# Optimization experiments

Measured on AMD Instinct MI355X. Metric: run time of the kernel, lower is better.

The kernel has to match this reference:

```python
import jax, jax.numpy as jnp
import numpy as np
import jax.lax as lax

EPS = 1e-5

def conv3x3(x, w):
    # x: [B,C,H,W], w: [O,C,3,3], stride 1, padding 1
    return lax.conv_general_dilated(x, w, (1, 1), ((1, 1), (1, 1)),
                                    dimension_numbers=('NCHW', 'OIHW', 'NCHW'))

def bn(x, s, b, m, v):
    inv = s / jnp.sqrt(v + EPS)
    return x * inv[None, :, None, None] + (b - m * inv)[None, :, None, None]

def conv_bn_relu(x, w, s, b, m, v):
    return jax.nn.relu(bn(conv3x3(x, w), s, b, m, v))

def spatial_attention(x, q_w, q_b, v_w, v_b, gamma):
    # Self_attention: q_conv used for both q and k (k_conv is dead in source)
    B, C, H, W = x.shape
    N = H * W
    q = (jnp.einsum('bchw,oc->bohw', x, q_w) + q_b[None, :, None, None]).reshape(B, -1, N)  # [B,Cq,N]
    v = (jnp.einsum('bchw,oc->bohw', x, v_w) + v_b[None, :, None, None]).reshape(B, C, N)   # [B,C,N]
    energy = jnp.einsum('bcn,bcm->bnm', q, q)          # [B,N,N]
    attn = jax.nn.softmax(energy, axis=-1)
    out = jnp.einsum('bcm,bnm->bcn', v, attn)          # v @ attn^T
    return gamma[0] * out.reshape(B, C, H, W) + x

def channel_attention(x, gamma):
    B, C, H, W = x.shape
    xf = x.reshape(B, C, -1)                           # [B,C,N]
    energy = jnp.einsum('bcn,bdn->bcd', xf, xf)        # [B,C,C]
    energy_new = jnp.max(energy, axis=-1, keepdims=True) - energy
    attn = jax.nn.softmax(energy_new, axis=-1)
    out = jnp.einsum('bcd,bdn->bcn', attn, xf)
    return gamma[0] * out.reshape(B, C, H, W) + x

def setup_inputs() -> dict:
    key = jax.random.key(0)
    ks = jax.random.split(key, 32)
    B, Cin, H, W = 4, 512, 64, 64
    Ci, Cq, Cout = 128, 16, 19
    f = jax.random.normal
    u = jax.random.uniform
    d = {}
    d['x'] = f(ks[0], (B, Cin, H, W), jnp.float32)
    d['conv5a_w'] = f(ks[1], (Ci, Cin, 3, 3), jnp.float32) * 0.02
    d['bn5a_s'] = u(ks[2], (Ci,), jnp.float32)
    d['bn5a_b'] = f(ks[3], (Ci,), jnp.float32) * 0.1
    d['bn5a_m'] = f(ks[4], (Ci,), jnp.float32) * 0.1
    d['bn5a_v'] = u(ks[5], (Ci,), jnp.float32) + 0.5
    d['conv5c_w'] = f(ks[6], (Ci, Cin, 3, 3), jnp.float32) * 0.02
    d['bn5c_s'] = u(ks[7], (Ci,), jnp.float32)
    d['bn5c_b'] = f(ks[8], (Ci,), jnp.float32) * 0.1
    d['bn5c_m'] = f(ks[9], (Ci,), jnp.float32) * 0.1
    d['bn5c_v'] = u(ks[10], (Ci,), jnp.float32) + 0.5
    d['q_w'] = f(ks[11], (Cq, Ci), jnp.float32) * 0.05
    d['q_b'] = f(ks[12], (Cq,), jnp.float32) * 0.05
    d['v_w'] = f(ks[13], (Ci, Ci), jnp.float32) * 0.05
    d['v_b'] = f(ks[14], (Ci,), jnp.float32) * 0.05
    d['gamma_sa'] = jnp.zeros((1,), jnp.float32)
    d['gamma_sc'] = jnp.zeros((1,), jnp.float32)
    d['conv51_w'] = f(ks[15], (Ci, Ci, 3, 3), jnp.float32) * 0.03
    d['bn51_s'] = u(ks[16], (Ci,), jnp.float32)
    d['bn51_b'] = f(ks[17], (Ci,), jnp.float32) * 0.1
    d['bn51_m'] = f(ks[18], (Ci,), jnp.float32) * 0.1
    d['bn51_v'] = u(ks[19], (Ci,), jnp.float32) + 0.5
    d['conv52_w'] = f(ks[20], (Ci, Ci, 3, 3), jnp.float32) * 0.03
    d['bn52_s'] = u(ks[21], (Ci,), jnp.float32)
    d['bn52_b'] = f(ks[22], (Ci,), jnp.float32) * 0.1
    d['bn52_m'] = f(ks[23], (Ci,), jnp.float32) * 0.1
    d['bn52_v'] = u(ks[24], (Ci,), jnp.float32) + 0.5
    d['conv8_w'] = f(ks[25], (Cout, Ci), jnp.float32) * 0.05
    d['conv8_b'] = f(ks[26], (Cout,), jnp.float32) * 0.05
    return d

def reference(x, conv5a_w, bn5a_s, bn5a_b, bn5a_m, bn5a_v,
              conv5c_w, bn5c_s, bn5c_b, bn5c_m, bn5c_v,
              q_w, q_b, v_w, v_b, gamma_sa, gamma_sc,
              conv51_w, bn51_s, bn51_b, bn51_m, bn51_v,
              conv52_w, bn52_s, bn52_b, bn52_m, bn52_v,
              conv8_w, conv8_b):
    feat1 = conv_bn_relu(x, conv5a_w, bn5a_s, bn5a_b, bn5a_m, bn5a_v)
    sa_feat = spatial_attention(feat1, q_w, q_b, v_w, v_b, gamma_sa)
    sa_conv = conv_bn_relu(sa_feat, conv51_w, bn51_s, bn51_b, bn51_m, bn51_v)
    feat2 = conv_bn_relu(x, conv5c_w, bn5c_s, bn5c_b, bn5c_m, bn5c_v)
    sc_feat = channel_attention(feat2, gamma_sc)
    sc_conv = conv_bn_relu(sc_feat, conv52_w, bn52_s, bn52_b, bn52_m, bn52_v)
    feat_sum = sa_conv + sc_conv
    # conv8 is a 1x1 conv (Dropout2d is identity in eval mode)
    out = jnp.einsum('bchw,oc->bohw', feat_sum, conv8_w) + conv8_b[None, :, None, None]
    return out
```

## Files before the change

### kernel.cpp

```cpp
#include <hip/hip_runtime.h>
#include <math.h>

#define EPS 1e-5f


typedef unsigned int uint;
typedef unsigned short u16;
typedef u16 u16x4 __attribute__((ext_vector_type(4)));
typedef u16 u16x8 __attribute__((ext_vector_type(8)));
typedef __bf16 bf16x8 __attribute__((ext_vector_type(8)));
typedef float f32x4 __attribute__((ext_vector_type(4)));
typedef float f32x16 __attribute__((ext_vector_type(16)));

#define WAIT_VM8() asm volatile("s_waitcnt vmcnt(8)" ::: "memory")
#define WAIT_VM0() asm volatile("s_waitcnt vmcnt(0)" ::: "memory")
#define BARRIER()  asm volatile("s_barrier" ::: "memory")

__device__ __forceinline__ u16 f2bf(float f) {
    uint u = __float_as_uint(f);
    u = u + 0x7FFF + ((u >> 16) & 1);
    return (u16)(u >> 16);
}
__device__ __forceinline__ float bf2f(u16 h) {
    return __uint_as_float(((uint)h) << 16);
}

__device__ __forceinline__ void gl_lds16(const void* g, void* l) {
    __builtin_amdgcn_global_load_lds(
        (const __attribute__((address_space(1))) unsigned int*)g,
        (__attribute__((address_space(3))) unsigned int*)l, 16, 0, 0);
}

__global__ void bn_prep_all(const float* s0, const float* b0, const float* m0, const float* v0,
                            const float* s1, const float* b1, const float* m1, const float* v1,
                            const float* s2, const float* b2, const float* m2, const float* v2,
                            const float* s3, const float* b3, const float* m3, const float* v3,
                            float* c0, float* c1, float* c2, float* c3) {
    int k = blockIdx.x, i = threadIdx.x;
    const float *s, *bb, *mm, *vv; float* cf;
    if (k == 0)      { s = s0; bb = b0; mm = m0; vv = v0; cf = c0; }
    else if (k == 1) { s = s1; bb = b1; mm = m1; vv = v1; cf = c1; }
    else if (k == 2) { s = s2; bb = b2; mm = m2; vv = v2; cf = c2; }
    else             { s = s3; bb = b3; mm = m3; vv = v3; cf = c3; }
    float inv = s[i] / sqrtf(vv[i] + EPS);
    cf[i] = inv;
    cf[128 + i] = bb[i] - mm[i] * inv;
}

__global__ void border_zero(u16* x0h, u16* x0l, u16* x1h, u16* x1l, u16* x2h, u16* x2l) {
    int p = blockIdx.x;
    int img = p / 260, pe = p % 260;
    int y, x;
    if (pe < 66)       { y = 0;  x = pe; }
    else if (pe < 132) { y = 65; x = pe - 66; }
    else { int q = pe - 132; y = 1 + (q >> 1); x = (q & 1) * 65; }
    int buf = blockIdx.y, tid = threadIdx.x;
    if (buf == 0) {
        size_t base = (((size_t)img * 66 + y) * 66 + x) * 512;
        for (int c = tid; c < 512; c += 256) { x0h[base + c] = 0; x0l[base + c] = 0; }
    } else {
        u16* hh = (buf == 1) ? x1h : x2h;
        u16* ll = (buf == 1) ? x1l : x2l;
        size_t base = (((size_t)img * 66 + y) * 66 + x) * 128;
        for (int c = tid; c < 128; c += 256) { hh[base + c] = 0; ll[base + c] = 0; }
    }
}

template <int CIN>
__global__ void pack_w(const float* __restrict__ w0, u16* __restrict__ h0, u16* __restrict__ l0,
                       const float* __restrict__ w1, u16* __restrict__ h1, u16* __restrict__ l1) {
    const float* w = blockIdx.z ? w1 : w0;
    u16* hh = blockIdx.z ? h1 : h0;
    u16* ll = blockIdx.z ? l1 : l0;
    int i = blockIdx.x * 256 + threadIdx.x;
    int ic = i & (CIN - 1);
    int rest = i / CIN;
    int oc = rest & 127;
    int tap = rest >> 7;
    float f = w[((size_t)oc * CIN + ic) * 9 + tap];
    u16 h = f2bf(f);
    hh[i] = h;
    ll[i] = f2bf(f - bf2f(h));
}

__global__ void pack_x(const float* __restrict__ x, u16* __restrict__ xh, u16* __restrict__ xl) {
    __shared__ float tile[64][68];
    int cb = blockIdx.x, y = blockIdx.y, b = blockIdx.z, tid = threadIdx.x;
    int cl = tid >> 2, seg = tid & 3;
    const float* src = x + (((size_t)b * 512 + cb * 64 + cl) * 64 + y) * 64 + seg * 16;
#pragma unroll
    for (int j = 0; j < 4; j++)
        *(f32x4*)&tile[cl][seg * 16 + j * 4] = *(const f32x4*)(src + j * 4);
    __syncthreads();
    int pxl = tid >> 2, cg = tid & 3;
    u16x8 h0, h1, l0, l1;
#pragma unroll
    for (int j = 0; j < 8; j++) {
        float v = tile[cg * 16 + j][pxl];
        u16 h = f2bf(v); h0[j] = h; l0[j] = f2bf(v - bf2f(h));
    }
#pragma unroll
    for (int j = 0; j < 8; j++) {
        float v = tile[cg * 16 + 8 + j][pxl];
        u16 h = f2bf(v); h1[j] = h; l1[j] = f2bf(v - bf2f(h));
    }
    size_t dst = (((size_t)b * 66 + y + 1) * 66 + (pxl + 1)) * 512 + cb * 64 + cg * 16;
    *(u16x8*)(xh + dst) = h0;  *(u16x8*)(xh + dst + 8) = h1;
    *(u16x8*)(xl + dst) = l0;  *(u16x8*)(xl + dst + 8) = l1;
}

template <int CIN, bool PACKOUT>
__launch_bounds__(256)
__global__ void conv_mfma(const u16* __restrict__ xh0, const u16* __restrict__ xl0,
                          const u16* __restrict__ xh1, const u16* __restrict__ xl1,
                          const u16* __restrict__ wh0, const u16* __restrict__ wl0,
                          const u16* __restrict__ wh1, const u16* __restrict__ wl1,
                          const float* __restrict__ coef0, const float* __restrict__ coef1,
                          float* __restrict__ fo0, float* __restrict__ fo1,
                          u16* __restrict__ ph0, u16* __restrict__ pl0,
                          u16* __restrict__ ph1, u16* __restrict__ pl1) {
    constexpr int ICC = CIN / 32;
    constexpr int NT  = 9 * ICC;
    const int z = blockIdx.z;
    const u16* xh = z ? xh1 : xh0;  const u16* xl = z ? xl1 : xl0;
    const u16* wh = z ? wh1 : wh0;  const u16* wl = z ? wl1 : wl0;
    const float* coef = z ? coef1 : coef0;
    float* fo = z ? fo1 : fo0;
    u16* ph = z ? ph1 : ph0;  u16* pl = z ? pl1 : pl0;

    const int tile = blockIdx.x;
    const int b  = tile >> 5;
    const int y0 = (tile & 31) * 2;
    const int tid = threadIdx.x;

    __shared__ char smem[65536];

    const int cidx = tid & 127;
    const int khv  = (tid >> 7) & 1;
    const u16* bAh = wh + (size_t)cidx * CIN + khv * 8;
    const u16* bAl = wl + (size_t)cidx * CIN + khv * 8;
    const int rr = cidx >> 6, xxc = cidx & 63;
    const size_t rowoff = ((size_t)(b * 66 + y0 + rr) * 66 + xxc) * CIN + khv * 8;
    const u16* bBh = xh + rowoff;
    const u16* bBl = xl + rowoff;
    char* ldst = smem + (tid & 192) * 16;

    const int wid = tid >> 6, lane = tid & 63;
    const int wr = wid >> 1, wc = wid & 1;
    const int l31 = lane & 31, lhi = lane >> 5;
    const int laneA = (lhi * 128 + wr * 64 + l31) * 16;
    const int laneB = 16384 + (lhi * 128 + wc * 64 + l31) * 16;

    f32x16 acc[2][2];
#pragma unroll
    for (int m = 0; m < 2; m++)
#pragma unroll
        for (int n = 0; n < 2; n++)
#pragma unroll
            for (int r = 0; r < 16; r++) acc[m][n][r] = 0.0f;

    auto stage = [&](int t, int db) {
        const int tap = t / ICC;
        const int ic0 = (t % ICC) * 32;
        const int offA = tap * 128 * CIN + ic0;
        const int offB = ((tap / 3) * 66 + (tap % 3)) * CIN + ic0;
        char* ld = ldst + db * 32768;
        gl_lds16(bAh + offA,      ld);
        gl_lds16(bAh + offA + 16, ld + 4096);
        gl_lds16(bAl + offA,      ld + 8192);
        gl_lds16(bAl + offA + 16, ld + 12288);
        gl_lds16(bBh + offB,      ld + 16384);
        gl_lds16(bBh + offB + 16, ld + 20480);
        gl_lds16(bBl + offB,      ld + 24576);
        gl_lds16(bBl + offB + 16, ld + 28672);
    };

    stage(0, 0);

    for (int t = 0; t < NT; ++t) {
        const int db = t & 1;
        if (t + 1 < NT) {
            stage(t + 1, db ^ 1);
            WAIT_VM8();
        } else {
            WAIT_VM0();
        }
        BARRIER();

        const char* sb = smem + db * 32768;

        bf16x8 Ah[2][2], Al[2][2], Bh[2][2], Bl[2][2];
#pragma unroll
        for (int kk = 0; kk < 2; kk++)
#pragma unroll
            for (int m = 0; m < 2; m++) {
                Ah[m][kk] = *(const bf16x8*)(sb + laneA + kk * 4096 + m * 512);
                Al[m][kk] = *(const bf16x8*)(sb + 8192 + laneA + kk * 4096 + m * 512);
            }
#pragma unroll
        for (int kk = 0; kk < 2; kk++)
#pragma unroll
            for (int n = 0; n < 2; n++) {
                Bh[n][kk] = *(const bf16x8*)(sb + laneB + kk * 4096 + n * 512);
                Bl[n][kk] = *(const bf16x8*)(sb + 8192 + laneB + kk * 4096 + n * 512);
            }
        __builtin_amdgcn_s_setprio(1);
#pragma unroll
        for (int m = 0; m < 2; m++)
#pragma unroll
            for (int n = 0; n < 2; n++)
#pragma unroll
                for (int kk = 0; kk < 2; kk++) {
                    acc[m][n] = __builtin_amdgcn_mfma_f32_32x32x16_bf16(Ah[m][kk], Bh[n][kk], acc[m][n], 0, 0, 0);
                    acc[m][n] = __builtin_amdgcn_mfma_f32_32x32x16_bf16(Ah[m][kk], Bl[n][kk], acc[m][n], 0, 0, 0);
                    acc[m][n] = __builtin_amdgcn_mfma_f32_32x32x16_bf16(Al[m][kk], Bh[n][kk], acc[m][n], 0, 0, 0);
                }
        __builtin_amdgcn_s_setprio(0);
        BARRIER();
    }

#pragma unroll
    for (int n = 0; n < 2; n++) {
        const int pxl = wc * 64 + n * 32 + l31;
        const int pxg = tile * 128 + pxl;
        const int bb = pxg >> 12, yy = (pxg >> 6) & 63, xg = pxg & 63;
        const size_t fbase = (size_t)pxg * 128;
        const size_t pbase = (((size_t)bb * 66 + yy + 1) * 66 + (xg + 1)) * 128;
#pragma unroll
        for (int m = 0; m < 2; m++)
#pragma unroll
            for (int q = 0; q < 4; q++) {
                const int oc4 = wr * 64 + m * 32 + q * 8 + lhi * 4;
                f32x4 sc = *(const f32x4*)&coef[oc4];
                f32x4 sh = *(const f32x4*)&coef[128 + oc4];
                f32x4 outv;
                u16x4 hv, lv;
#pragma unroll
                for (int j = 0; j < 4; j++) {
                    float v = acc[m][n][q * 4 + j] * sc[j] + sh[j];
                    v = v > 0.0f ? v : 0.0f;
                    outv[j] = v;
                    if (PACKOUT) {
                        u16 h = f2bf(v);
                        hv[j] = h;
                        lv[j] = f2bf(v - bf2f(h));
                    }
                }
                *(f32x4*)&fo[fbase + oc4] = outv;
                if (PACKOUT) {
                    *(u16x4*)&ph[pbase + oc4] = hv;
                    *(u16x4*)&pl[pbase + oc4] = lv;
                }
            }
    }
}

__launch_bounds__(256)
__global__ void conv1x1(const float* __restrict__ fa, const float* __restrict__ fb,
                        const float* __restrict__ w8, const float* __restrict__ b8,
                        float* __restrict__ out) {
    __shared__ float s_w[128 * 20];
    int tid = threadIdx.x;
    for (int i = tid; i < 19 * 128; i += 256) {
        int o = i >> 7, c = i & 127;
        s_w[c * 20 + o] = w8[i];
    }
    __syncthreads();
    size_t px = (size_t)blockIdx.x * 256 + tid;
    const f32x4* A = (const f32x4*)(fa + px * 128);
    const f32x4* B = (const f32x4*)(fb + px * 128);
    float acc[19];
#pragma unroll
    for (int o = 0; o < 19; o++) acc[o] = 0.0f;
    for (int cq = 0; cq < 32; cq++) {
        f32x4 v = A[cq] + B[cq];
#pragma unroll
        for (int j = 0; j < 4; j++) {
            float iv = v[j];
            int c = cq * 4 + j;
#pragma unroll
            for (int o = 0; o < 19; o++) acc[o] += iv * s_w[c * 20 + o];
        }
    }
    int b = px >> 12, n = px & 4095;
#pragma unroll
    for (int o = 0; o < 19; o++)
        out[((size_t)b * 19 + o) * 4096 + n] = acc[o] + b8[o];
}


__global__ void lin_q(const float* __restrict__ g, const float* __restrict__ feat,
                      const float* __restrict__ qw, const float* __restrict__ qb,
                      float* __restrict__ outq) {
    if (g[0] == 0.0f) return;
    __shared__ float s_w[16 * 128];
    int tid = threadIdx.x;
    for (int i = tid; i < 2048; i += 256) s_w[i] = qw[i];
    __syncthreads();
    size_t px = (size_t)blockIdx.x * 256 + tid;
    const float* in = feat + px * 128;
    float acc[16];
#pragma unroll
    for (int o = 0; o < 16; o++) acc[o] = 0.0f;
    for (int c = 0; c < 128; c++) {
        float iv = in[c];
#pragma unroll
        for (int o = 0; o < 16; o++) acc[o] += iv * s_w[o * 128 + c];
    }
#pragma unroll
    for (int o = 0; o < 16; o++) outq[px * 16 + o] = acc[o] + qb[o];
}

__global__ void lin_v(const float* __restrict__ g, const float* __restrict__ feat,
                      const float* __restrict__ vw, const float* __restrict__ vb,
                      float* __restrict__ outv) {
    if (g[0] == 0.0f) return;
    int tid = threadIdx.x;
    size_t px = (size_t)blockIdx.x * 64 + (tid >> 2);
    int q4 = tid & 3;
    const float* in = feat + px * 128;
    float acc[32];
#pragma unroll
    for (int j = 0; j < 32; j++) acc[j] = 0.0f;
    for (int c = 0; c < 128; c++) {
        float iv = in[c];
        for (int j = 0; j < 32; j++) acc[j] += iv * vw[(size_t)(q4 * 32 + j) * 128 + c];
    }
    for (int j = 0; j < 32; j++)
        outv[px * 128 + q4 * 32 + j] = acc[j] + vb[q4 * 32 + j];
}

__global__ void sa_attn(const float* __restrict__ g, const float* __restrict__ qb,
                        const float* __restrict__ vb, const float* __restrict__ feat1,
                        u16* __restrict__ ph, u16* __restrict__ pl) {
    if (g[0] == 0.0f) return;
    float gamma = g[0];
    int b = blockIdx.y, grp = blockIdx.x, tid = threadIdx.x;
    __shared__ float s_e[4096];
    __shared__ float s_red[256];
    __shared__ float s_q[16];
    __shared__ float s_o[256];
    for (int ni = 0; ni < 32; ni++) {
        int n = grp * 32 + ni;
        if (tid < 16) s_q[tid] = qb[((size_t)b * 4096 + n) * 16 + tid];
        __syncthreads();
        float lmax = -1e30f;
        for (int m = tid; m < 4096; m += 256) {
            const float* qm = qb + ((size_t)b * 4096 + m) * 16;
            float e = 0.0f;
#pragma unroll
            for (int k = 0; k < 16; k++) e += s_q[k] * qm[k];
            s_e[m] = e;
            lmax = fmaxf(lmax, e);
        }
        s_red[tid] = lmax;
        __syncthreads();
        for (int s = 128; s > 0; s >>= 1) {
            if (tid < s) s_red[tid] = fmaxf(s_red[tid], s_red[tid + s]);
            __syncthreads();
        }
        float mx = s_red[0];
        __syncthreads();
        float lsum = 0.0f;
        for (int m = tid; m < 4096; m += 256) {
            float p = expf(s_e[m] - mx);
            s_e[m] = p;
            lsum += p;
        }
        s_red[tid] = lsum;
        __syncthreads();
        for (int s = 128; s > 0; s >>= 1) {
            if (tid < s) s_red[tid] += s_red[tid + s];
            __syncthreads();
        }
        float denom = s_red[0];
        __syncthreads();
        int c = tid & 127, half = tid >> 7;
        float acc = 0.0f;
        for (int m = half * 2048; m < half * 2048 + 2048; m++)
            acc += s_e[m] * vb[((size_t)b * 4096 + m) * 128 + c];
        s_o[tid] = acc;
        __syncthreads();
        if (tid < 128) {
            float o = (s_o[tid] + s_o[tid + 128]) / denom;
            float val = feat1[((size_t)b * 4096 + n) * 128 + tid] + gamma * o;
            int yy = n >> 6, xx = n & 63;
            size_t pidx = (((size_t)b * 66 + yy + 1) * 66 + (xx + 1)) * 128 + tid;
            u16 h = f2bf(val);
            ph[pidx] = h;
            pl[pidx] = f2bf(val - bf2f(h));
        }
        __syncthreads();
    }
}

__global__ void ca_attn(const float* __restrict__ g, const float* __restrict__ feat2,
                        u16* __restrict__ ph, u16* __restrict__ pl) {
    if (g[0] == 0.0f) return;
    float gamma = g[0];
    int b = blockIdx.y, crow = blockIdx.x, d = threadIdx.x;
    __shared__ float s_red[128];
    __shared__ float s_attn[128];
    const float* base = feat2 + (size_t)b * 4096 * 128;
    float e = 0.0f;
    for (int n = 0; n < 4096; n++) e += base[(size_t)n * 128 + crow] * base[(size_t)n * 128 + d];
    s_red[d] = e;
    __syncthreads();
    for (int s = 64; s > 0; s >>= 1) {
        if (d < s) s_red[d] = fmaxf(s_red[d], s_red[d + s]);
        __syncthreads();
    }
    float m1 = s_red[0];
    __syncthreads();
    float en = m1 - e;
    s_red[d] = en;
    __syncthreads();
    for (int s = 64; s > 0; s >>= 1) {
        if (d < s) s_red[d] = fmaxf(s_red[d], s_red[d + s]);
        __syncthreads();
    }
    float m2 = s_red[0];
    __syncthreads();
    float p = expf(en - m2);
    s_red[d] = p;
    __syncthreads();
    for (int s = 64; s > 0; s >>= 1) {
        if (d < s) s_red[d] += s_red[d + s];
        __syncthreads();
    }
    s_attn[d] = p / s_red[0];
    __syncthreads();
    for (int n = d; n < 4096; n += 128) {
        float acc = 0.0f;
#pragma unroll 8
        for (int dd = 0; dd < 128; dd++) acc += s_attn[dd] * base[(size_t)n * 128 + dd];
        float val = base[(size_t)n * 128 + crow] + gamma * acc;
        int yy = n >> 6, xx = n & 63;
        size_t pidx = (((size_t)b * 66 + yy + 1) * 66 + (xx + 1)) * 128 + crow;
        u16 h = f2bf(val);
        ph[pidx] = h;
        pl[pidx] = f2bf(val - bf2f(h));
    }
}

extern "C" void kernel_launch(void* const* d_in, const int* in_sizes, int n_in,
                              void* d_out, int out_size, void* d_ws, size_t ws_size,
                              hipStream_t stream) {
    const float* x      = (const float*)d_in[0];
    const float* w5a    = (const float*)d_in[1];
    const float* bn5a_s = (const float*)d_in[2];
    const float* bn5a_b = (const float*)d_in[3];
    const float* bn5a_m = (const float*)d_in[4];
    const float* bn5a_v = (const float*)d_in[5];
    const float* w5c    = (const float*)d_in[6];
    const float* bn5c_s = (const float*)d_in[7];
    const float* bn5c_b = (const float*)d_in[8];
    const float* bn5c_m = (const float*)d_in[9];
    const float* bn5c_v = (const float*)d_in[10];
    const float* q_w    = (const float*)d_in[11];
    const float* q_b    = (const float*)d_in[12];
    const float* v_w    = (const float*)d_in[13];
    const float* v_b    = (const float*)d_in[14];
    const float* g_sa   = (const float*)d_in[15];
    const float* g_sc   = (const float*)d_in[16];
    const float* w51    = (const float*)d_in[17];
    const float* bn51_s = (const float*)d_in[18];
    const float* bn51_b = (const float*)d_in[19];
    const float* bn51_m = (const float*)d_in[20];
    const float* bn51_v = (const float*)d_in[21];
    const float* w52    = (const float*)d_in[22];
    const float* bn52_s = (const float*)d_in[23];
    const float* bn52_b = (const float*)d_in[24];
    const float* bn52_m = (const float*)d_in[25];
    const float* bn52_v = (const float*)d_in[26];
    const float* w8     = (const float*)d_in[27];
    const float* b8     = (const float*)d_in[28];
    float* out = (float*)d_out;
    (void)in_sizes; (void)n_in; (void)out_size; (void)ws_size;

    char* W = (char*)d_ws;
    constexpr size_t XP0 = (size_t)4 * 66 * 66 * 512 * 2;
    constexpr size_t XP1 = (size_t)4 * 66 * 66 * 128 * 2;
    constexpr size_t WPA = (size_t)9 * 128 * 512 * 2;
    constexpr size_t WPB = (size_t)9 * 128 * 128 * 2;
    constexpr size_t FT  = (size_t)4 * 4096 * 128 * 4;
    size_t off = 0;
    u16* xp0h = (u16*)(W + off); off += XP0;
    u16* xp0l = (u16*)(W + off); off += XP0;
    u16* xp1h = (u16*)(W + off); off += XP1;
    u16* xp1l = (u16*)(W + off); off += XP1;
    u16* xp2h = (u16*)(W + off); off += XP1;
    u16* xp2l = (u16*)(W + off); off += XP1;
    u16* wp5ah = (u16*)(W + off); off += WPA;
    u16* wp5al = (u16*)(W + off); off += WPA;
    u16* wp5ch = (u16*)(W + off); off += WPA;
    u16* wp5cl = (u16*)(W + off); off += WPA;
    u16* wp51h = (u16*)(W + off); off += WPB;
    u16* wp51l = (u16*)(W + off); off += WPB;
    u16* wp52h = (u16*)(W + off); off += WPB;
    u16* wp52l = (u16*)(W + off); off += WPB;
    float* c5a = (float*)(W + off); off += 1024;
    float* c5c = (float*)(W + off); off += 1024;
    float* c51 = (float*)(W + off); off += 1024;
    float* c52 = (float*)(W + off); off += 1024;
    float* b0  = (float*)(W + off); off += FT;
    float* b1  = (float*)(W + off); off += FT;
    float* b3a = (float*)(W + off); off += FT;
    float* b3b = (float*)(W + off); off += FT;
    float* qbuf = b3a;
    float* vbuf = (float*)((char*)b3a + 1048576);

    border_zero<<<dim3(1040, 3), 256, 0, stream>>>(xp0h, xp0l, xp1h, xp1l, xp2h, xp2l);
    bn_prep_all<<<4, 128, 0, stream>>>(bn5a_s, bn5a_b, bn5a_m, bn5a_v,
                                       bn5c_s, bn5c_b, bn5c_m, bn5c_v,
                                       bn51_s, bn51_b, bn51_m, bn51_v,
                                       bn52_s, bn52_b, bn52_m, bn52_v,
                                       c5a, c5c, c51, c52);
    pack_w<512><<<dim3(2304, 1, 2), 256, 0, stream>>>(w5a, wp5ah, wp5al, w5c, wp5ch, wp5cl);
    pack_w<128><<<dim3(576, 1, 2), 256, 0, stream>>>(w51, wp51h, wp51l, w52, wp52h, wp52l);
    pack_x<<<dim3(8, 64, 4), 256, 0, stream>>>(x, xp0h, xp0l);

    conv_mfma<512, true><<<dim3(128, 1, 2), 256, 0, stream>>>(
        xp0h, xp0l, xp0h, xp0l,
        wp5ah, wp5al, wp5ch, wp5cl,
        c5a, c5c, b0, b1,
        xp1h, xp1l, xp2h, xp2l);

    lin_q<<<64, 256, 0, stream>>>(g_sa, b0, q_w, q_b, qbuf);
    lin_v<<<256, 256, 0, stream>>>(g_sa, b0, v_w, v_b, vbuf);
    sa_attn<<<dim3(128, 4), 256, 0, stream>>>(g_sa, qbuf, vbuf, b0, xp1h, xp1l);
    ca_attn<<<dim3(128, 4), 128, 0, stream>>>(g_sc, b1, xp2h, xp2l);

    conv_mfma<128, false><<<dim3(128, 1, 2), 256, 0, stream>>>(
        xp1h, xp1l, xp2h, xp2l,
        wp51h, wp51l, wp52h, wp52l,
        c51, c52, b3a, b3b,
        nullptr, nullptr, nullptr, nullptr);

    conv1x1<<<64, 256, 0, stream>>>(b3a, b3b, w8, b8, out);
}
```

Measured before the change: 364.6 us.

## Triple-buffer conv LDS pipeline and remap block indices across batch and branch

The conv MFMA kernel now uses three LDS stages with prefetch distance two, waiting on vmcnt(16), to hide more global-load latency. The 3D grid is flattened into a 1D grid whose block index interleaves batch and branch, which changes how tiles spread across CUs and caches. LDS per block grows to 96KB, which could limit occupancy if more than one block per CU were desired.

```diff
diff --git a/kernel.cpp b/kernel.cpp
--- a/kernel.cpp
+++ b/kernel.cpp
@@ -12,9 +12,10 @@
 typedef float f32x4 __attribute__((ext_vector_type(4)));
 typedef float f32x16 __attribute__((ext_vector_type(16)));
 
-#define WAIT_VM8() asm volatile("s_waitcnt vmcnt(8)" ::: "memory")
-#define WAIT_VM0() asm volatile("s_waitcnt vmcnt(0)" ::: "memory")
-#define BARRIER()  asm volatile("s_barrier" ::: "memory")
+#define WAIT_VM16() asm volatile("s_waitcnt vmcnt(16)" ::: "memory")
+#define WAIT_VM8()  asm volatile("s_waitcnt vmcnt(8)" ::: "memory")
+#define WAIT_VM0()  asm volatile("s_waitcnt vmcnt(0)" ::: "memory")
+#define BARRIER()   asm volatile("s_barrier" ::: "memory")
 
 __device__ __forceinline__ u16 f2bf(float f) {
     uint u = __float_as_uint(f);
@@ -121,19 +122,21 @@
                           u16* __restrict__ ph1, u16* __restrict__ pl1) {
     constexpr int ICC = CIN / 32;
     constexpr int NT  = 9 * ICC;
-    const int z = blockIdx.z;
+    const int bid = blockIdx.x;
+    const int z  = (bid >> 2) & 1;
+    const int b  = bid & 3;
+    const int y0 = (bid >> 3) * 2;
+    const int tile = b * 32 + (bid >> 3);
+
     const u16* xh = z ? xh1 : xh0;  const u16* xl = z ? xl1 : xl0;
     const u16* wh = z ? wh1 : wh0;  const u16* wl = z ? wl1 : wl0;
     const float* coef = z ? coef1 : coef0;
     float* fo = z ? fo1 : fo0;
     u16* ph = z ? ph1 : ph0;  u16* pl = z ? pl1 : pl0;
 
-    const int tile = blockIdx.x;
-    const int b  = tile >> 5;
-    const int y0 = (tile & 31) * 2;
     const int tid = threadIdx.x;
 
-    __shared__ char smem[65536];
+    __shared__ char smem[98304];
 
     const int cidx = tid & 127;
     const int khv  = (tid >> 7) & 1;
@@ -159,12 +162,12 @@
 #pragma unroll
             for (int r = 0; r < 16; r++) acc[m][n][r] = 0.0f;
 
-    auto stage = [&](int t, int db) {
+    auto stage = [&](int t, int buf) {
         const int tap = t / ICC;
         const int ic0 = (t % ICC) * 32;
         const int offA = tap * 128 * CIN + ic0;
         const int offB = ((tap / 3) * 66 + (tap % 3)) * CIN + ic0;
-        char* ld = ldst + db * 32768;
+        char* ld = ldst + buf * 32768;
         gl_lds16(bAh + offA,      ld);
         gl_lds16(bAh + offA + 16, ld + 4096);
         gl_lds16(bAl + offA,      ld + 8192);
@@ -176,18 +179,22 @@
     };
 
     stage(0, 0);
-
+    stage(1, 1);
+
+    int buf = 0;
+    int hb  = 2;
     for (int t = 0; t < NT; ++t) {
-        const int db = t & 1;
-        if (t + 1 < NT) {
-            stage(t + 1, db ^ 1);
+        if (t + 2 < NT) {
+            stage(t + 2, hb);
+            WAIT_VM16();
+        } else if (t + 1 < NT) {
             WAIT_VM8();
         } else {
             WAIT_VM0();
         }
         BARRIER();
 
-        const char* sb = smem + db * 32768;
+        const char* sb = smem + buf * 32768;
 
         bf16x8 Ah[2][2], Al[2][2], Bh[2][2], Bl[2][2];
 #pragma unroll
@@ -217,6 +224,9 @@
                 }
         __builtin_amdgcn_s_setprio(0);
         BARRIER();
+
+        buf = buf + 1; if (buf == 3) buf = 0;
+        hb  = hb + 1;  if (hb == 3)  hb = 0;
     }
 
 #pragma unroll
@@ -520,7 +530,7 @@
     pack_w<128><<<dim3(576, 1, 2), 256, 0, stream>>>(w51, wp51h, wp51l, w52, wp52h, wp52l);
     pack_x<<<dim3(8, 64, 4), 256, 0, stream>>>(x, xp0h, xp0l);
 
-    conv_mfma<512, true><<<dim3(128, 1, 2), 256, 0, stream>>>(
+    conv_mfma<512, true><<<256, 256, 0, stream>>>(
         xp0h, xp0l, xp0h, xp0l,
         wp5ah, wp5al, wp5ch, wp5cl,
         c5a, c5c, b0, b1,
@@ -531,7 +541,7 @@
     sa_attn<<<dim3(128, 4), 256, 0, stream>>>(g_sa, qbuf, vbuf, b0, xp1h, xp1l);
     ca_attn<<<dim3(128, 4), 128, 0, stream>>>(g_sc, b1, xp2h, xp2l);
 
-    conv_mfma<128, false><<<dim3(128, 1, 2), 256, 0, stream>>>(
+    conv_mfma<128, false><<<256, 256, 0, stream>>>(
         xp1h, xp1l, xp2h, xp2l,
         wp51h, wp51l, wp52h, wp52l,
         c51, c52, b3a, b3b,
```

Result: slower. 380.0 us (+4.2%).
